# Optimization experiments

Hardware: AMD Instinct MI355X
Metric: run time of the kernel (lower is better)

## Reference

```python
import jax, jax.numpy as jnp
import numpy as np

B, N, DIM, HEADS, DH, EDGE, DEPTH, K = 4, 128, 256, 8, 64, 64, 2, 512
INNER = HEADS * DH
SCALE = DH ** -0.5


def _ln(x, g, b, eps=1e-5):
    m = x.mean(-1, keepdims=True)
    v = ((x - m) ** 2).mean(-1, keepdims=True)
    return (x - m) / jnp.sqrt(v + eps) * g + b


def _rotate_half(x):
    # interleaved pairs: (d r) with r=2 -> (-x2, x1)
    xp = x.reshape(x.shape[:-1] + (-1, 2))
    x1, x2 = xp[..., 0], xp[..., 1]
    return jnp.stack((-x2, x1), axis=-1).reshape(x.shape)


def _gated_res(x, res, gw):
    gate = jax.nn.sigmoid(jnp.concatenate((x, res, x - res), axis=-1) @ gw)
    return x * gate + res * (1 - gate)


def forward(nodes, edges, edge_ln_g, edge_ln_b, ln1_g, ln1_b, w_exp, b_exp,
            w_q, b_q, w_kv, b_kv, w_ekv, b_ekv, w_out, b_out, gate1_w,
            ln2_g, ln2_b, w_ff1, b_ff1, w_ff2, b_ff2, gate2_w, codebook):
    b, n = nodes.shape[:2]
    # LayerNorm edges over channel dim: (B,C,N,N) -> (B,N,N,C)
    e = _ln(jnp.transpose(edges, (0, 2, 3, 1)), edge_ln_g, edge_ln_b)
    # rotary frequencies over positions, repeated pairwise -> (1, N, DH)
    inv = 1.0 / (10000.0 ** (jnp.arange(0, DH, 2, dtype=jnp.float32) / DH))
    fr = jnp.repeat(jnp.arange(n, dtype=jnp.float32)[:, None] * inv[None, :], 2, axis=-1)
    cos, sin = jnp.cos(fr)[None], jnp.sin(fr)[None]

    def heads3(t):  # (B,N,H*D) -> (B*H,N,D)
        return t.reshape(b, n, HEADS, DH).transpose(0, 2, 1, 3).reshape(b * HEADS, n, DH)

    for i in range(DEPTH):
        # PreNorm + edge-conditioned attention
        x = _ln(nodes, ln1_g[i], ln1_b[i])
        x = x @ w_exp[i] + b_exp[i]
        q = x @ w_q[i] + b_q[i]
        k, v = jnp.split(x @ w_kv[i] + b_kv[i], 2, axis=-1)
        ekv = e @ w_ekv[i] + b_ekv[i]  # (B,N,N,INNER)
        q, k, v = heads3(q), heads3(k), heads3(v)
        ekv = ekv.reshape(b, n, n, HEADS, DH).transpose(0, 3, 1, 2, 4).reshape(b * HEADS, n, n, DH)
        q = q * cos + _rotate_half(q) * sin
        k = k * cos + _rotate_half(k) * sin
        kk = k[:, None, :, :] + ekv  # (BH, i, j, d)
        vv = v[:, None, :, :] + ekv
        sim = jnp.einsum('bid,bijd->bij', q, kk) * SCALE
        att = jax.nn.softmax(sim, axis=-1)
        out = jnp.einsum('bij,bijd->bid', att, vv)
        out = out.reshape(b, HEADS, n, DH).transpose(0, 2, 1, 3).reshape(b, n, INNER)
        out = out @ w_out[i] + b_out[i]
        nodes = _gated_res(out, nodes, gate1_w[i])
        # PreNorm + FeedForward
        h = _ln(nodes, ln2_g[i], ln2_b[i])
        h = jax.nn.gelu(h @ w_ff1[i] + b_ff1[i], approximate=False) @ w_ff2[i] + b_ff2[i]
        nodes = _gated_res(h, nodes, gate2_w[i])

    # VQ codebook nearest-neighbor lookup with straight-through estimator
    z = nodes.reshape(-1, DIM)
    d = (z * z).sum(-1, keepdims=True) - 2.0 * z @ codebook.T + (codebook * codebook).sum(-1)[None, :]
    idx = jnp.argmin(d, axis=-1)
    zq = codebook[idx].reshape(b, n, DIM)
    return nodes + jax.lax.stop_gradient(zq - nodes)


def setup_inputs() -> dict:
    key = jax.random.key(0)
    ks = jax.random.split(key, 16)
    s = 0.02
    inp = {
        'nodes': jax.random.normal(ks[0], (B, N, DIM), jnp.float32),
        'edges': jax.random.normal(ks[1], (B, EDGE, N, N), jnp.float32),
        'edge_ln_g': jnp.ones((EDGE,), jnp.float32),
        'edge_ln_b': jnp.zeros((EDGE,), jnp.float32),
        'ln1_g': jnp.ones((DEPTH, DIM), jnp.float32),
        'ln1_b': jnp.zeros((DEPTH, DIM), jnp.float32),
        'w_exp': s * jax.random.normal(ks[2], (DEPTH, DIM, INNER), jnp.float32),
        'b_exp': jnp.zeros((DEPTH, INNER), jnp.float32),
        'w_q': s * jax.random.normal(ks[3], (DEPTH, INNER, INNER), jnp.float32),
        'b_q': jnp.zeros((DEPTH, INNER), jnp.float32),
        'w_kv': s * jax.random.normal(ks[4], (DEPTH, INNER, 2 * INNER), jnp.float32),
        'b_kv': jnp.zeros((DEPTH, 2 * INNER), jnp.float32),
        'w_ekv': s * jax.random.normal(ks[5], (DEPTH, EDGE, INNER), jnp.float32),
        'b_ekv': jnp.zeros((DEPTH, INNER), jnp.float32),
        'w_out': s * jax.random.normal(ks[6], (DEPTH, INNER, DIM), jnp.float32),
        'b_out': jnp.zeros((DEPTH, DIM), jnp.float32),
        'gate1_w': s * jax.random.normal(ks[7], (DEPTH, 3 * DIM, 1), jnp.float32),
        'ln2_g': jnp.ones((DEPTH, DIM), jnp.float32),
        'ln2_b': jnp.zeros((DEPTH, DIM), jnp.float32),
        'w_ff1': s * jax.random.normal(ks[8], (DEPTH, DIM, 4 * DIM), jnp.float32),
        'b_ff1': jnp.zeros((DEPTH, 4 * DIM), jnp.float32),
        'w_ff2': s * jax.random.normal(ks[9], (DEPTH, 4 * DIM, DIM), jnp.float32),
        'b_ff2': jnp.zeros((DEPTH, DIM), jnp.float32),
        'gate2_w': s * jax.random.normal(ks[10], (DEPTH, 3 * DIM, 1), jnp.float32),
        'codebook': jax.random.uniform(ks[11], (K, DIM), jnp.float32, -1.0 / K, 1.0 / K),
    }
    return inp


def reference(nodes, edges, edge_ln_g, edge_ln_b, ln1_g, ln1_b, w_exp, b_exp,
              w_q, b_q, w_kv, b_kv, w_ekv, b_ekv, w_out, b_out, gate1_w,
              ln2_g, ln2_b, w_ff1, b_ff1, w_ff2, b_ff2, gate2_w, codebook):
    return forward(nodes, edges, edge_ln_g, edge_ln_b, ln1_g, ln1_b, w_exp, b_exp,
                   w_q, b_q, w_kv, b_kv, w_ekv, b_ekv, w_out, b_out, gate1_w,
                   ln2_g, ln2_b, w_ff1, b_ff1, w_ff2, b_ff2, gate2_w, codebook)
```

## Files before the change

### kernel.cpp

```cpp
#include <hip/hip_runtime.h>
#include <math.h>


#define DEV __device__ __forceinline__

constexpr int Bn = 4, Nn = 128, DIMn = 256, HEADSn = 8, DHn = 64, EDGEn = 64,
              DEPTHn = 2, Kn = 512, INNERn = 512;
constexpr int QKVW = 1536;
constexpr int PART = 131072;

DEV float wave_reduce_sum(float v) {
#pragma unroll
  for (int m = 32; m >= 1; m >>= 1) v += __shfl_xor(v, m);
  return v;
}

DEV float block_reduce_sum_256(float v, float* red) {
  v = wave_reduce_sum(v);
  int tid = threadIdx.x;
  if ((tid & 63) == 0) red[tid >> 6] = v;
  __syncthreads();
  v = red[0] + red[1] + red[2] + red[3];
  __syncthreads();
  return v;
}

DEV float gelu_exact(float x) {
  return 0.5f * x * (1.f + erff(x * 0.70710678118654752f));
}

__global__ __launch_bounds__(256) void prep_kernel(
    const float* __restrict__ edges, const float* __restrict__ eg,
    const float* __restrict__ eb, float* __restrict__ e,
    float* __restrict__ eT, float* __restrict__ cost, float* __restrict__ sint,
    const float* __restrict__ nodes_in, const float* __restrict__ ln1_g,
    const float* __restrict__ ln1_b, float* __restrict__ xln,
    float* __restrict__ nodes, const float* __restrict__ wek,
    const float* __restrict__ w_out, const float* __restrict__ bek,
    const float* __restrict__ b_out, float* __restrict__ W2,
    float* __restrict__ b_out2, const float* __restrict__ w_exp,
    const float* __restrict__ b_exp, const float* __restrict__ w_q,
    const float* __restrict__ b_q, const float* __restrict__ w_kv,
    const float* __restrict__ b_kv, float* __restrict__ WqkvF,
    float* __restrict__ bqkvF) {
  __shared__ float smem[8512];
  int blk = blockIdx.x;
  int tid = threadIdx.x;

  if (blk < 64) {
    int l = blk >> 5, h = (blk >> 2) & 7, nt = blk & 3;
    float* As = smem;
    float* Bs = smem + 4160;
    const float* wekl = wek + (size_t)l * 64 * 512 + h * 64;
    const float* woutl =
        w_out + (size_t)l * 512 * 256 + (size_t)(h * 64) * 256 + nt * 64;
    for (int f = tid; f < 1024; f += 256) {
      int c = f >> 4, d4 = (f & 15) << 2;
      float4 w4 = *(const float4*)(wekl + (size_t)c * 512 + d4);
      As[c * 65 + d4 + 0] = w4.x;
      As[c * 65 + d4 + 1] = w4.y;
      As[c * 65 + d4 + 2] = w4.z;
      As[c * 65 + d4 + 3] = w4.w;
    }
    for (int f = tid; f < 1024; f += 256) {
      int d = f >> 4, n4 = (f & 15) << 2;
      float4 w4 = *(const float4*)(woutl + (size_t)d * 256 + n4);
      Bs[d * 68 + n4 + 0] = w4.x;
      Bs[d * 68 + n4 + 1] = w4.y;
      Bs[d * 68 + n4 + 2] = w4.z;
      Bs[d * 68 + n4 + 3] = w4.w;
    }
    __syncthreads();
    int tx = tid & 15, ty = tid >> 4;
    float acc[4][4] = {};
    for (int d = 0; d < 64; ++d) {
      float4 bv = *(const float4*)&Bs[d * 68 + tx * 4];
#pragma unroll
      for (int u = 0; u < 4; ++u) {
        float a = As[(ty * 4 + u) * 65 + d];
        acc[u][0] += a * bv.x;
        acc[u][1] += a * bv.y;
        acc[u][2] += a * bv.z;
        acc[u][3] += a * bv.w;
      }
    }
#pragma unroll
    for (int u = 0; u < 4; ++u) {
      float4 o = {acc[u][0], acc[u][1], acc[u][2], acc[u][3]};
      *(float4*)(W2 + (size_t)l * 512 * 256 +
                 (size_t)(h * 64 + ty * 4 + u) * 256 + nt * 64 + tx * 4) = o;
    }
  } else if (blk < 72) {
    int t = blk - 64;
    int l = t >> 2, nt = t & 3;
    float* part = smem;
    int nn = tid & 63, kq = tid >> 6;
    const float* wcol = w_out + (size_t)l * 512 * 256 + nt * 64 + nn;
    float acc = 0.f;
    for (int k = kq * 128; k < kq * 128 + 128; ++k)
      acc += bek[l * 512 + k] * wcol[(size_t)k * 256];
    part[tid] = acc;
    __syncthreads();
    if (tid < 64)
      b_out2[l * 256 + nt * 64 + nn] =
          b_out[l * 256 + nt * 64 + nn] + part[nn] + part[64 + nn] +
          part[128 + nn] + part[192 + nn];
  } else if (blk < 584) {
    float* ets = smem;
    int eidx = blk - 72;
    int i = eidx & 127, b = eidx >> 7;
    int j = tid & 127;
    bool act = tid < 128;
    if (act) {
      const float* src = edges + (size_t)b * EDGEn * Nn * Nn + i * Nn + j;
      float vals[EDGEn];
      float s = 0.f;
#pragma unroll
      for (int c = 0; c < EDGEn; ++c) {
        float x = src[(size_t)c * (Nn * Nn)];
        vals[c] = x;
        s += x;
      }
      float m = s * (1.0f / 64.0f);
      float s2 = 0.f;
#pragma unroll
      for (int c = 0; c < EDGEn; ++c) {
        float d = vals[c] - m;
        s2 += d * d;
      }
      float inv = 1.f / sqrtf(s2 * (1.0f / 64.0f) + 1e-5f);
      float* dst = e + ((size_t)(b * Nn + i) * EDGEn) * Nn + j;
#pragma unroll
      for (int c = 0; c < EDGEn; ++c) {
        float o = (vals[c] - m) * inv * eg[c] + eb[c];
        dst[(size_t)c * Nn] = o;
        ets[j * 65 + c] = o;
      }
    }
    __syncthreads();
    if (act) {
      float* dstT = eT + ((size_t)(b * Nn + i) * Nn) * EDGEn;
#pragma unroll
      for (int it = 0; it < 16; ++it) {
        int f4 = it * 128 + j;
        int jj = f4 >> 4, c4 = (f4 & 15) << 2;
        float4 o4 = {ets[jj * 65 + c4], ets[jj * 65 + c4 + 1],
                     ets[jj * 65 + c4 + 2], ets[jj * 65 + c4 + 3]};
        *(float4*)(dstT + (size_t)jj * EDGEn + c4) = o4;
      }
    }
  } else if (blk < 600) {
    int t = (blk - 584) * 256 + tid;
    if (t < Nn * 32) {
      int n = t >> 5, p = t & 31;
      float inv = powf(10000.f, -(float)(2 * p) / 64.f);
      float fr = (float)n * inv;
      cost[t] = cosf(fr);
      sint[t] = sinf(fr);
    }
  } else if (blk < 1112) {
    float* red = smem;
    int row = blk - 600;
    float v = nodes_in[(size_t)row * DIMn + tid];
    nodes[(size_t)row * DIMn + tid] = v;
    float m = block_reduce_sum_256(v, red) * (1.0f / 256.0f);
    float d = v - m;
    float var = block_reduce_sum_256(d * d, red) * (1.0f / 256.0f);
    float inv = 1.f / sqrtf(var + 1e-5f);
    xln[(size_t)row * DIMn + tid] = d * inv * ln1_g[tid] + ln1_b[tid];
  } else if (blk < 1496) {
    int t = blk - 1112;
    int l = t / 192, r = t % 192;
    int by = r / 24, bx = r % 24;
    float* As = smem;
    float* Bs = smem + 32 * 34;
    int n0 = bx * 64;
    const float* Aab = w_exp + (size_t)l * 256 * 512 + (size_t)(by * 32) * 512;
    const float* Wb;
    int ldw;
    if (n0 < 512) {
      Wb = w_q + (size_t)l * 512 * 512 + n0;
      ldw = 512;
    } else {
      Wb = w_kv + (size_t)l * 512 * 1024 + (n0 - 512);
      ldw = 1024;
    }
    int arow = tid >> 3, acol = (tid & 7) << 2;
    int brow = tid >> 4, bcol = (tid & 15) << 2;
    int tx = tid & 15, ty = tid >> 4;
    float acc[2][4] = {};
    for (int k0 = 0; k0 < 512; k0 += 32) {
      float4 a4 = *(const float4*)(Aab + (size_t)arow * 512 + k0 + acol);
      As[(acol + 0) * 34 + arow] = a4.x;
      As[(acol + 1) * 34 + arow] = a4.y;
      As[(acol + 2) * 34 + arow] = a4.z;
      As[(acol + 3) * 34 + arow] = a4.w;
      *(float4*)&Bs[brow * 68 + bcol] =
          *(const float4*)(Wb + (size_t)(k0 + brow) * ldw + bcol);
      *(float4*)&Bs[(brow + 16) * 68 + bcol] =
          *(const float4*)(Wb + (size_t)(k0 + brow + 16) * ldw + bcol);
      __syncthreads();
#pragma unroll
      for (int kk = 0; kk < 32; ++kk) {
        float2 av = *(const float2*)&As[kk * 34 + ty * 2];
        float4 bv = *(const float4*)&Bs[kk * 68 + tx * 4];
        acc[0][0] += av.x * bv.x;
        acc[0][1] += av.x * bv.y;
        acc[0][2] += av.x * bv.z;
        acc[0][3] += av.x * bv.w;
        acc[1][0] += av.y * bv.x;
        acc[1][1] += av.y * bv.y;
        acc[1][2] += av.y * bv.z;
        acc[1][3] += av.y * bv.w;
      }
      __syncthreads();
    }
#pragma unroll
    for (int u = 0; u < 2; ++u) {
      int d = by * 32 + ty * 2 + u;
      float4 o = {acc[u][0], acc[u][1], acc[u][2], acc[u][3]};
      *(float4*)(WqkvF + (size_t)l * 256 * 1536 + (size_t)d * 1536 + n0 +
                 tx * 4) = o;
    }
  } else {
    int t = blk - 1496;
    int l = t / 6, seg = t % 6;
    int n = seg * 256 + tid;
    const float* W;
    int ldw;
    float acc;
    if (n < 512) {
      W = w_q + (size_t)l * 512 * 512 + n;
      ldw = 512;
      acc = b_q[l * 512 + n];
    } else {
      W = w_kv + (size_t)l * 512 * 1024 + (n - 512);
      ldw = 1024;
      acc = b_kv[l * 1024 + (n - 512)];
    }
    const float* be = b_exp + l * 512;
    for (int k = 0; k < 512; ++k) acc += be[k] * W[(size_t)k * ldw];
    bqkvF[l * 1536 + n] = acc;
  }
}

__global__ __launch_bounds__(256) void gemm_kernel(
    const float* __restrict__ A, const float* __restrict__ A2, int aact,
    const float* __restrict__ W1, int N1, const float* __restrict__ b1,
    const float* __restrict__ W2n, int N2, const float* __restrict__ b2,
    const float* __restrict__ Wkb, int Ksplit, float* __restrict__ C, int M,
    int Ntot, int K, int kspan, int act, const float* __restrict__ cost,
    const float* __restrict__ sint, float* __restrict__ kT) {
  __shared__ float As[32][34];
  __shared__ __align__(16) float Bs[32][68];
  int tid = threadIdx.x;
  int bx = blockIdx.x, by = blockIdx.y, zid = blockIdx.z;
  int tx = tid & 15, ty = tid >> 4;
  int arow = tid >> 3, acol = (tid & 7) << 2;
  int brow = tid >> 4, bcol = (tid & 15) << 2;
  int col0 = bx * 64;
  const float* W = W1;
  const float* bias = b1;
  int Nw = N1, wcol = col0;
  if (W2n && col0 >= N1) {
    W = W2n;
    bias = b2;
    Nw = N2;
    wcol = col0 - N1;
  }
  int kb = zid * kspan, kend = kb + kspan;
  const float* arp = A + (size_t)(by * 32 + arow) * K;
  const float* arp2 = A2 ? A2 + (size_t)(by * 32 + arow) * K : nullptr;

  auto load_a = [&](int kpos) -> float4 {
    float4 a = *(const float4*)(arp + kpos + acol);
    if (arp2) {
      float4 a2 = *(const float4*)(arp2 + kpos + acol);
      a.x += a2.x;
      a.y += a2.y;
      a.z += a2.z;
      a.w += a2.w;
    }
    if (aact == 1) {
      a.x = gelu_exact(a.x);
      a.y = gelu_exact(a.y);
      a.z = gelu_exact(a.z);
      a.w = gelu_exact(a.w);
    }
    return a;
  };

  float4 a_nxt = load_a(kb);
  const float* w0p;
  const float* w1p;
  {
    int kr0 = kb + brow, kr1 = kb + brow + 16;
    w0p = (Ksplit && kr0 >= Ksplit)
              ? Wkb + (size_t)(kr0 - Ksplit) * Nw + wcol + bcol
              : W + (size_t)kr0 * Nw + wcol + bcol;
    w1p = (Ksplit && kr1 >= Ksplit)
              ? Wkb + (size_t)(kr1 - Ksplit) * Nw + wcol + bcol
              : W + (size_t)kr1 * Nw + wcol + bcol;
  }
  float4 b0_nxt = *(const float4*)w0p;
  float4 b1_nxt = *(const float4*)w1p;

  float acc[2][4] = {};
  for (int k0 = kb; k0 < kend; k0 += 32) {
    As[acol + 0][arow] = a_nxt.x;
    As[acol + 1][arow] = a_nxt.y;
    As[acol + 2][arow] = a_nxt.z;
    As[acol + 3][arow] = a_nxt.w;
    *(float4*)&Bs[brow][bcol] = b0_nxt;
    *(float4*)&Bs[brow + 16][bcol] = b1_nxt;
    __syncthreads();
    int kn = k0 + 32;
    if (kn < kend) {
      a_nxt = load_a(kn);
      int kr0 = kn + brow, kr1 = kn + brow + 16;
      w0p = (Ksplit && kr0 >= Ksplit)
                ? Wkb + (size_t)(kr0 - Ksplit) * Nw + wcol + bcol
                : W + (size_t)kr0 * Nw + wcol + bcol;
      w1p = (Ksplit && kr1 >= Ksplit)
                ? Wkb + (size_t)(kr1 - Ksplit) * Nw + wcol + bcol
                : W + (size_t)kr1 * Nw + wcol + bcol;
      b0_nxt = *(const float4*)w0p;
      b1_nxt = *(const float4*)w1p;
    }
#pragma unroll
    for (int kk = 0; kk < 32; ++kk) {
      float2 av = *(const float2*)&As[kk][ty * 2];
      float4 bv = *(const float4*)&Bs[kk][tx * 4];
      acc[0][0] += av.x * bv.x;
      acc[0][1] += av.x * bv.y;
      acc[0][2] += av.x * bv.z;
      acc[0][3] += av.x * bv.w;
      acc[1][0] += av.y * bv.x;
      acc[1][1] += av.y * bv.y;
      acc[1][2] += av.y * bv.z;
      acc[1][3] += av.y * bv.w;
    }
    __syncthreads();
  }
  int ccol = wcol + tx * 4;
  bool ksec = (act == 4) && (col0 >= 512) && (col0 < 1024);
  float* trans = (float*)Bs;
  float* Cz = C + (size_t)zid * M * Ntot;
#pragma unroll
  for (int u = 0; u < 2; ++u) {
    int r = by * 32 + ty * 2 + u;
    float o[4];
#pragma unroll
    for (int w = 0; w < 4; ++w)
      o[w] = acc[u][w] + (zid == 0 ? bias[ccol + w] : 0.f);
    if (act == 1) {
#pragma unroll
      for (int w = 0; w < 4; ++w) o[w] = gelu_exact(o[w]);
    } else if (act == 4 && col0 < 1024) {
      int n = r & 127;
      int p0 = (ccol & 63) >> 1;
      float c0 = cost[n * 32 + p0], s0 = sint[n * 32 + p0];
      float c1 = cost[n * 32 + p0 + 1], s1 = sint[n * 32 + p0 + 1];
      float x0 = o[0], x1 = o[1], x2 = o[2], x3 = o[3];
      o[0] = x0 * c0 - x1 * s0;
      o[1] = x1 * c0 + x0 * s0;
      o[2] = x2 * c1 - x3 * s1;
      o[3] = x3 * c1 + x2 * s1;
    }
    if (ksec) {
#pragma unroll
      for (int w = 0; w < 4; ++w) trans[(tx * 4 + w) * 33 + ty * 2 + u] = o[w];
    } else {
      float4 o4 = {o[0], o[1], o[2], o[3]};
      *(float4*)(Cz + (size_t)r * Ntot + col0 + tx * 4) = o4;
    }
  }
  if (ksec) {
    __syncthreads();
    int h = (col0 - 512) >> 6;
    int bb = (by * 32) >> 7;
#pragma unroll
    for (int q = 0; q < 2; ++q) {
      int f4 = tid * 2 + q;
      int dl = f4 >> 3, j4 = (f4 & 7) << 2;
      int jj = (by * 32 + j4) & 127;
      float4 o4 = {trans[dl * 33 + j4], trans[dl * 33 + j4 + 1],
                   trans[dl * 33 + j4 + 2], trans[dl * 33 + j4 + 3]};
      *(float4*)(kT + ((size_t)(bb * 8 + h) * 64 + dl) * 128 + jj) = o4;
    }
  }
}

__global__ __launch_bounds__(128) void attn_kernel(
    const float* __restrict__ qkv, const float* __restrict__ e,
    const float* __restrict__ eT, const float* __restrict__ kT,
    const float* __restrict__ wek, const float* __restrict__ w_out,
    const float* __restrict__ W2, float* __restrict__ proj) {
  __shared__ __align__(16) float qs[256];
  __shared__ __align__(16) float qes[256];
  __shared__ __align__(16) float att[512];
  __shared__ float avh[512];
  __shared__ float aeh[512];
  __shared__ float wekh[64 * 65];
  int blk = blockIdx.x;
  int iq = blk & 31;
  int bh = blk >> 5;
  int h = bh & 7, b = bh >> 3;
  int i0 = iq * 4;
  int row0 = b * 128 + i0;
  int tid = threadIdx.x;

  for (int f = tid; f < 256; f += 128) {
    int ii = f >> 6, d = f & 63;
    qs[f] = qkv[(size_t)(row0 + ii) * QKVW + h * 64 + d];
  }
  for (int f = tid; f < 4096; f += 128) {
    int c = f >> 6, d = f & 63;
    wekh[c * 65 + d] = wek[(size_t)c * INNERn + h * 64 + d];
  }
  __syncthreads();

  for (int f = tid; f < 256; f += 128) {
    int ii = f >> 6, c = f & 63;
    float acc = 0.f;
#pragma unroll
    for (int d = 0; d < 64; ++d) acc += qs[ii * 64 + d] * wekh[c * 65 + d];
    qes[f] = acc;
  }
  __syncthreads();

  int i2 = tid >> 5, j4 = tid & 31;
  float s0 = 0.f, s1 = 0.f, s2 = 0.f, s3 = 0.f;
  {
    const float* ktb = kT + ((size_t)bh * 64) * 128 + j4 * 4;
#pragma unroll
    for (int d4 = 0; d4 < 64; d4 += 4) {
      float4 q4 = *(const float4*)&qs[i2 * 64 + d4];
      float4 k0 = *(const float4*)(ktb + (size_t)(d4 + 0) * 128);
      float4 k1 = *(const float4*)(ktb + (size_t)(d4 + 1) * 128);
      float4 k2 = *(const float4*)(ktb + (size_t)(d4 + 2) * 128);
      float4 k3 = *(const float4*)(ktb + (size_t)(d4 + 3) * 128);
      s0 += q4.x * k0.x + q4.y * k1.x + q4.z * k2.x + q4.w * k3.x;
      s1 += q4.x * k0.y + q4.y * k1.y + q4.z * k2.y + q4.w * k3.y;
      s2 += q4.x * k0.z + q4.y * k1.z + q4.z * k2.z + q4.w * k3.z;
      s3 += q4.x * k0.w + q4.y * k1.w + q4.z * k2.w + q4.w * k3.w;
    }
    const float* eb = e + ((size_t)(row0 + i2) * 64) * 128 + j4 * 4;
#pragma unroll
    for (int c4 = 0; c4 < 64; c4 += 4) {
      float4 qe4 = *(const float4*)&qes[i2 * 64 + c4];
      float4 e0 = *(const float4*)(eb + (size_t)(c4 + 0) * 128);
      float4 e1 = *(const float4*)(eb + (size_t)(c4 + 1) * 128);
      float4 e2 = *(const float4*)(eb + (size_t)(c4 + 2) * 128);
      float4 e3 = *(const float4*)(eb + (size_t)(c4 + 3) * 128);
      s0 += qe4.x * e0.x + qe4.y * e1.x + qe4.z * e2.x + qe4.w * e3.x;
      s1 += qe4.x * e0.y + qe4.y * e1.y + qe4.z * e2.y + qe4.w * e3.y;
      s2 += qe4.x * e0.z + qe4.y * e1.z + qe4.z * e2.z + qe4.w * e3.z;
      s3 += qe4.x * e0.w + qe4.y * e1.w + qe4.z * e2.w + qe4.w * e3.w;
    }
    s0 *= 0.125f;
    s1 *= 0.125f;
    s2 *= 0.125f;
    s3 *= 0.125f;
  }
  {
    float mx = fmaxf(fmaxf(s0, s1), fmaxf(s2, s3));
#pragma unroll
    for (int m = 16; m >= 1; m >>= 1) mx = fmaxf(mx, __shfl_xor(mx, m));
    float p0 = expf(s0 - mx), p1 = expf(s1 - mx), p2 = expf(s2 - mx),
          p3 = expf(s3 - mx);
    float sm = p0 + p1 + p2 + p3;
#pragma unroll
    for (int m = 16; m >= 1; m >>= 1) sm += __shfl_xor(sm, m);
    float inv = 1.f / sm;
    float4 a4 = {p0 * inv, p1 * inv, p2 * inv, p3 * inv};
    *(float4*)&att[i2 * 128 + j4 * 4] = a4;
  }
  __syncthreads();

  {
    int d = tid & 63, half = tid >> 6;
    float av0 = 0.f, av1 = 0.f, av2 = 0.f, av3 = 0.f;
    float ae0 = 0.f, ae1 = 0.f, ae2 = 0.f, ae3 = 0.f;
    const float* vb = qkv + (size_t)(b * 128) * QKVW + 1024 + h * 64 + d;
    const float* etb = eT + ((size_t)row0 * 128) * 64 + d;
    for (int jq = 0; jq < 16; ++jq) {
      int jb = half * 64 + jq * 4;
      float4 a0 = *(const float4*)&att[0 * 128 + jb];
      float4 a1 = *(const float4*)&att[1 * 128 + jb];
      float4 a2 = *(const float4*)&att[2 * 128 + jb];
      float4 a3 = *(const float4*)&att[3 * 128 + jb];
#pragma unroll
      for (int t = 0; t < 4; ++t) {
        int j = jb + t;
        float vv = vb[(size_t)j * QKVW];
        float at0 = ((const float*)&a0)[t];
        float at1 = ((const float*)&a1)[t];
        float at2 = ((const float*)&a2)[t];
        float at3 = ((const float*)&a3)[t];
        av0 += at0 * vv;
        av1 += at1 * vv;
        av2 += at2 * vv;
        av3 += at3 * vv;
        float e0 = etb[(size_t)j * 64];
        float e1 = etb[8192 + (size_t)j * 64];
        float e2 = etb[16384 + (size_t)j * 64];
        float e3 = etb[24576 + (size_t)j * 64];
        ae0 += at0 * e0;
        ae1 += at1 * e1;
        ae2 += at2 * e2;
        ae3 += at3 * e3;
      }
    }
    avh[half * 256 + 0 * 64 + d] = av0;
    avh[half * 256 + 1 * 64 + d] = av1;
    avh[half * 256 + 2 * 64 + d] = av2;
    avh[half * 256 + 3 * 64 + d] = av3;
    aeh[half * 256 + 0 * 64 + d] = ae0;
    aeh[half * 256 + 1 * 64 + d] = ae1;
    aeh[half * 256 + 2 * 64 + d] = ae2;
    aeh[half * 256 + 3 * 64 + d] = ae3;
  }
  __syncthreads();

  for (int f = tid; f < 256; f += 128) {
    int ii = f >> 6, dd = f & 63;
    att[ii * 128 + dd] = avh[ii * 64 + dd] + avh[256 + ii * 64 + dd];
    att[ii * 128 + 64 + dd] = aeh[ii * 64 + dd] + aeh[256 + ii * 64 + dd];
  }
  __syncthreads();

  {
    int rp = tid >> 6, n4 = (tid & 63) << 2;
    int r0 = rp * 2, r1 = rp * 2 + 1;
    float o0[4] = {}, o1[4] = {};
    const float* wo = w_out + (size_t)(h * 64) * 256 + n4;
#pragma unroll 8
    for (int k = 0; k < 64; ++k) {
      float4 w4 = *(const float4*)(wo + (size_t)k * 256);
      float a0 = att[r0 * 128 + k];
      float a1 = att[r1 * 128 + k];
      o0[0] += a0 * w4.x;
      o0[1] += a0 * w4.y;
      o0[2] += a0 * w4.z;
      o0[3] += a0 * w4.w;
      o1[0] += a1 * w4.x;
      o1[1] += a1 * w4.y;
      o1[2] += a1 * w4.z;
      o1[3] += a1 * w4.w;
    }
    const float* w2 = W2 + (size_t)(h * 64) * 256 + n4;
#pragma unroll 8
    for (int k = 0; k < 64; ++k) {
      float4 w4 = *(const float4*)(w2 + (size_t)k * 256);
      float a0 = att[r0 * 128 + 64 + k];
      float a1 = att[r1 * 128 + 64 + k];
      o0[0] += a0 * w4.x;
      o0[1] += a0 * w4.y;
      o0[2] += a0 * w4.z;
      o0[3] += a0 * w4.w;
      o1[0] += a1 * w4.x;
      o1[1] += a1 * w4.y;
      o1[2] += a1 * w4.z;
      o1[3] += a1 * w4.w;
    }
    float* pp = proj + (size_t)h * PART;
    float4 v0 = {o0[0], o0[1], o0[2], o0[3]};
    float4 v1 = {o1[0], o1[1], o1[2], o1[3]};
    *(float4*)(pp + (size_t)(row0 + r0) * 256 + n4) = v0;
    *(float4*)(pp + (size_t)(row0 + r1) * 256 + n4) = v1;
  }
}

__global__ __launch_bounds__(256) void gate_ln_kernel(
    const float* __restrict__ x, int nparts, const float* __restrict__ badd,
    float* __restrict__ nodes, const float* __restrict__ gw,
    const float* __restrict__ lng, const float* __restrict__ lnb,
    float* __restrict__ xln) {
  __shared__ float red[4];
  int row = blockIdx.x, tid = threadIdx.x;
  size_t off = (size_t)row * DIMn + tid;
  float xv = x[off];
  for (int p = 1; p < nparts; ++p) xv += x[off + (size_t)p * PART];
  if (badd) xv += badd[tid];
  float rv = nodes[off];
  float pv =
      xv * gw[tid] + rv * gw[DIMn + tid] + (xv - rv) * gw[2 * DIMn + tid];
  float ssum = block_reduce_sum_256(pv, red);
  float gsig = 1.f / (1.f + expf(-ssum));
  float nv = xv * gsig + rv * (1.f - gsig);
  nodes[off] = nv;
  if (lng) {
    float m = block_reduce_sum_256(nv, red) * (1.0f / 256.0f);
    float d = nv - m;
    float var = block_reduce_sum_256(d * d, red) * (1.0f / 256.0f);
    float inv = 1.f / sqrtf(var + 1e-5f);
    xln[off] = d * inv * lng[tid] + lnb[tid];
  }
}

__global__ __launch_bounds__(256) void vq_kernel(
    const float* __restrict__ nodes, const float* __restrict__ codebook,
    float* __restrict__ out) {
  __shared__ __align__(16) float zs[4 * 256];
  __shared__ float wval[4][4];
  __shared__ int widx[4][4];
  __shared__ int fidx[4];
  int row0 = blockIdx.x * 4;
  int tid = threadIdx.x;
  for (int f = tid; f < 1024; f += 256) zs[f] = nodes[(size_t)row0 * DIMn + f];
  __syncthreads();
  int k1 = tid, k2 = tid + 256;
  const float4* c1p = (const float4*)(codebook + (size_t)k1 * DIMn);
  const float4* c2p = (const float4*)(codebook + (size_t)k2 * DIMn);
  float dot[4][2] = {};
  float cc0 = 0.f, cc1 = 0.f;
#pragma unroll 8
  for (int d4 = 0; d4 < 64; ++d4) {
    float4 c1 = c1p[d4], c2 = c2p[d4];
    cc0 += c1.x * c1.x + c1.y * c1.y + c1.z * c1.z + c1.w * c1.w;
    cc1 += c2.x * c2.x + c2.y * c2.y + c2.z * c2.z + c2.w * c2.w;
#pragma unroll
    for (int r = 0; r < 4; ++r) {
      float4 z = *(const float4*)&zs[r * 256 + d4 * 4];
      dot[r][0] += c1.x * z.x + c1.y * z.y + c1.z * z.z + c1.w * z.w;
      dot[r][1] += c2.x * z.x + c2.y * z.y + c2.z * z.z + c2.w * z.w;
    }
  }
  int lane = tid & 63, w = tid >> 6;
#pragma unroll
  for (int r = 0; r < 4; ++r) {
    float bv = cc0 - 2.f * dot[r][0];
    int bi = k1;
    float v2 = cc1 - 2.f * dot[r][1];
    if (v2 < bv) {
      bv = v2;
      bi = k2;
    }
#pragma unroll
    for (int m = 32; m >= 1; m >>= 1) {
      float ov = __shfl_xor(bv, m);
      int oi = __shfl_xor(bi, m);
      if (ov < bv || (ov == bv && oi < bi)) {
        bv = ov;
        bi = oi;
      }
    }
    if (lane == 0) {
      wval[r][w] = bv;
      widx[r][w] = bi;
    }
  }
  __syncthreads();
  if (tid < 4) {
    float bb = wval[tid][0];
    int bi = widx[tid][0];
    for (int t = 1; t < 4; ++t)
      if (wval[tid][t] < bb || (wval[tid][t] == bb && widx[tid][t] < bi)) {
        bb = wval[tid][t];
        bi = widx[tid][t];
      }
    fidx[tid] = bi;
  }
  __syncthreads();
  for (int f = tid; f < 1024; f += 256) {
    int r = f >> 8, d = f & 255;
    float zv = zs[f];
    float zq = codebook[(size_t)fidx[r] * DIMn + d];
    out[(size_t)(row0 + r) * DIMn + d] = zv + (zq - zv);
  }
}

extern "C" void kernel_launch(void* const* d_in, const int* in_sizes, int n_in,
                              void* d_out, int out_size, void* d_ws,
                              size_t ws_size, hipStream_t stream) {
  const float* nodes_in = (const float*)d_in[0];
  const float* edges = (const float*)d_in[1];
  const float* edge_ln_g = (const float*)d_in[2];
  const float* edge_ln_b = (const float*)d_in[3];
  const float* ln1_g = (const float*)d_in[4];
  const float* ln1_b = (const float*)d_in[5];
  const float* w_exp = (const float*)d_in[6];
  const float* b_exp = (const float*)d_in[7];
  const float* w_q = (const float*)d_in[8];
  const float* b_q = (const float*)d_in[9];
  const float* w_kv = (const float*)d_in[10];
  const float* b_kv = (const float*)d_in[11];
  const float* w_ekv = (const float*)d_in[12];
  const float* b_ekv = (const float*)d_in[13];
  const float* w_out = (const float*)d_in[14];
  const float* b_out = (const float*)d_in[15];
  const float* gate1_w = (const float*)d_in[16];
  const float* ln2_g = (const float*)d_in[17];
  const float* ln2_b = (const float*)d_in[18];
  const float* w_ff1 = (const float*)d_in[19];
  const float* b_ff1 = (const float*)d_in[20];
  const float* w_ff2 = (const float*)d_in[21];
  const float* b_ff2 = (const float*)d_in[22];
  const float* gate2_w = (const float*)d_in[23];
  const float* codebook = (const float*)d_in[24];

  float* ws = (float*)d_ws;
  float* e_buf = ws;
  float* eT_buf = e_buf + 4194304;
  float* cost = eT_buf + 4194304;
  float* sint = cost + 4096;
  float* nodes = sint + 4096;
  float* xln = nodes + 131072;
  float* qkvb = xln + 131072;
  float* kTb = qkvb + 786432;
  float* proj = kTb + 262144;
  float* ff1 = proj + 1048576;
  float* W2buf = ff1 + 1048576;
  float* bout2 = W2buf + 262144;
  float* WqkvF = bout2 + 512;
  float* bqkvF = WqkvF + 786432;

  prep_kernel<<<1508, 256, 0, stream>>>(
      edges, edge_ln_g, edge_ln_b, e_buf, eT_buf, cost, sint, nodes_in, ln1_g,
      ln1_b, xln, nodes, w_ekv, w_out, b_ekv, b_out, W2buf, bout2, w_exp,
      b_exp, w_q, b_q, w_kv, b_kv, WqkvF, bqkvF);

  for (int l = 0; l < DEPTHn; ++l) {
    gemm_kernel<<<dim3(24, 16, 1), 256, 0, stream>>>(
        xln, nullptr, 0, WqkvF + (size_t)l * 256 * 1536, 1536,
        bqkvF + l * 1536, nullptr, 0, nullptr, nullptr, 0, qkvb, 512, QKVW,
        256, 256, 4, cost, sint, kTb);
    attn_kernel<<<1024, 128, 0, stream>>>(qkvb, e_buf, eT_buf, kTb,
                                          w_ekv + l * 64 * 512,
                                          w_out + l * 512 * 256,
                                          W2buf + l * 512 * 256, proj);
    gate_ln_kernel<<<512, 256, 0, stream>>>(
        proj, 8, bout2 + l * 256, nodes, gate1_w + l * 768, ln2_g + l * 256,
        ln2_b + l * 256, xln);
    gemm_kernel<<<dim3(16, 16, 2), 256, 0, stream>>>(
        xln, nullptr, 0, w_ff1 + l * 256 * 1024, 1024, b_ff1 + l * 1024,
        nullptr, 0, nullptr, nullptr, 0, ff1, 512, 1024, 256, 128, 0, cost,
        sint, nullptr);
    gemm_kernel<<<dim3(4, 16, 4), 256, 0, stream>>>(
        ff1, ff1 + 524288, 1, w_ff2 + l * 1024 * 256, 256, b_ff2 + l * 256,
        nullptr, 0, nullptr, nullptr, 0, proj, 512, 256, 1024, 256, 0, cost,
        sint, nullptr);
    const float* nlng = (l + 1 < DEPTHn) ? ln1_g + (l + 1) * 256 : nullptr;
    const float* nlnb = (l + 1 < DEPTHn) ? ln1_b + (l + 1) * 256 : nullptr;
    gate_ln_kernel<<<512, 256, 0, stream>>>(proj, 4, nullptr, nodes,
                                            gate2_w + l * 768, nlng, nlnb,
                                            xln);
  }
  vq_kernel<<<128, 256, 0, stream>>>(nodes, codebook, (float*)d_out);
}
```

Before: 338.0 us.

## Reorder prep kernel blocks, shrink shared memory, prefetch weight-fold GEMM tiles

The prep kernel's heterogeneous block roles are reordered so the long serial bias-fold and weight-fold GEMM blocks launch first and the short LayerNorm blocks run last. Shared memory per block drops from about 34KB to about 18KB by chunking the edge transpose and the W2 fold into 32-wide pieces, which should let more blocks stay resident per CU. The fused weight GEMM now register-prefetches the next k-tile of global loads while computing on the current one. The costs are extra barriers in the chunked loops and more live registers for the prefetch.

After: 319.0 us. -5.6%, faster.

```diff
diff --git a/kernel.cpp b/kernel.cpp
--- a/kernel.cpp
+++ b/kernel.cpp
@@ -43,133 +43,32 @@
     const float* __restrict__ b_q, const float* __restrict__ w_kv,
     const float* __restrict__ b_kv, float* __restrict__ WqkvF,
     float* __restrict__ bqkvF) {
-  __shared__ float smem[8512];
+  __shared__ __align__(16) float smem[4480];
   int blk = blockIdx.x;
   int tid = threadIdx.x;
 
-  if (blk < 64) {
-    int l = blk >> 5, h = (blk >> 2) & 7, nt = blk & 3;
-    float* As = smem;
-    float* Bs = smem + 4160;
-    const float* wekl = wek + (size_t)l * 64 * 512 + h * 64;
-    const float* woutl =
-        w_out + (size_t)l * 512 * 256 + (size_t)(h * 64) * 256 + nt * 64;
-    for (int f = tid; f < 1024; f += 256) {
-      int c = f >> 4, d4 = (f & 15) << 2;
-      float4 w4 = *(const float4*)(wekl + (size_t)c * 512 + d4);
-      As[c * 65 + d4 + 0] = w4.x;
-      As[c * 65 + d4 + 1] = w4.y;
-      As[c * 65 + d4 + 2] = w4.z;
-      As[c * 65 + d4 + 3] = w4.w;
-    }
-    for (int f = tid; f < 1024; f += 256) {
-      int d = f >> 4, n4 = (f & 15) << 2;
-      float4 w4 = *(const float4*)(woutl + (size_t)d * 256 + n4);
-      Bs[d * 68 + n4 + 0] = w4.x;
-      Bs[d * 68 + n4 + 1] = w4.y;
-      Bs[d * 68 + n4 + 2] = w4.z;
-      Bs[d * 68 + n4 + 3] = w4.w;
-    }
-    __syncthreads();
-    int tx = tid & 15, ty = tid >> 4;
-    float acc[4][4] = {};
-    for (int d = 0; d < 64; ++d) {
-      float4 bv = *(const float4*)&Bs[d * 68 + tx * 4];
-#pragma unroll
-      for (int u = 0; u < 4; ++u) {
-        float a = As[(ty * 4 + u) * 65 + d];
-        acc[u][0] += a * bv.x;
-        acc[u][1] += a * bv.y;
-        acc[u][2] += a * bv.z;
-        acc[u][3] += a * bv.w;
-      }
-    }
-#pragma unroll
-    for (int u = 0; u < 4; ++u) {
-      float4 o = {acc[u][0], acc[u][1], acc[u][2], acc[u][3]};
-      *(float4*)(W2 + (size_t)l * 512 * 256 +
-                 (size_t)(h * 64 + ty * 4 + u) * 256 + nt * 64 + tx * 4) = o;
-    }
-  } else if (blk < 72) {
-    int t = blk - 64;
-    int l = t >> 2, nt = t & 3;
-    float* part = smem;
-    int nn = tid & 63, kq = tid >> 6;
-    const float* wcol = w_out + (size_t)l * 512 * 256 + nt * 64 + nn;
-    float acc = 0.f;
-    for (int k = kq * 128; k < kq * 128 + 128; ++k)
-      acc += bek[l * 512 + k] * wcol[(size_t)k * 256];
-    part[tid] = acc;
-    __syncthreads();
-    if (tid < 64)
-      b_out2[l * 256 + nt * 64 + nn] =
-          b_out[l * 256 + nt * 64 + nn] + part[nn] + part[64 + nn] +
-          part[128 + nn] + part[192 + nn];
-  } else if (blk < 584) {
-    float* ets = smem;
-    int eidx = blk - 72;
-    int i = eidx & 127, b = eidx >> 7;
-    int j = tid & 127;
-    bool act = tid < 128;
-    if (act) {
-      const float* src = edges + (size_t)b * EDGEn * Nn * Nn + i * Nn + j;
-      float vals[EDGEn];
-      float s = 0.f;
-#pragma unroll
-      for (int c = 0; c < EDGEn; ++c) {
-        float x = src[(size_t)c * (Nn * Nn)];
-        vals[c] = x;
-        s += x;
-      }
-      float m = s * (1.0f / 64.0f);
-      float s2 = 0.f;
-#pragma unroll
-      for (int c = 0; c < EDGEn; ++c) {
-        float d = vals[c] - m;
-        s2 += d * d;
-      }
-      float inv = 1.f / sqrtf(s2 * (1.0f / 64.0f) + 1e-5f);
-      float* dst = e + ((size_t)(b * Nn + i) * EDGEn) * Nn + j;
-#pragma unroll
-      for (int c = 0; c < EDGEn; ++c) {
-        float o = (vals[c] - m) * inv * eg[c] + eb[c];
-        dst[(size_t)c * Nn] = o;
-        ets[j * 65 + c] = o;
-      }
-    }
-    __syncthreads();
-    if (act) {
-      float* dstT = eT + ((size_t)(b * Nn + i) * Nn) * EDGEn;
-#pragma unroll
-      for (int it = 0; it < 16; ++it) {
-        int f4 = it * 128 + j;
-        int jj = f4 >> 4, c4 = (f4 & 15) << 2;
-        float4 o4 = {ets[jj * 65 + c4], ets[jj * 65 + c4 + 1],
-                     ets[jj * 65 + c4 + 2], ets[jj * 65 + c4 + 3]};
-        *(float4*)(dstT + (size_t)jj * EDGEn + c4) = o4;
-      }
-    }
-  } else if (blk < 600) {
-    int t = (blk - 584) * 256 + tid;
-    if (t < Nn * 32) {
-      int n = t >> 5, p = t & 31;
-      float inv = powf(10000.f, -(float)(2 * p) / 64.f);
-      float fr = (float)n * inv;
-      cost[t] = cosf(fr);
-      sint[t] = sinf(fr);
-    }
-  } else if (blk < 1112) {
-    float* red = smem;
-    int row = blk - 600;
-    float v = nodes_in[(size_t)row * DIMn + tid];
-    nodes[(size_t)row * DIMn + tid] = v;
-    float m = block_reduce_sum_256(v, red) * (1.0f / 256.0f);
-    float d = v - m;
-    float var = block_reduce_sum_256(d * d, red) * (1.0f / 256.0f);
-    float inv = 1.f / sqrtf(var + 1e-5f);
-    xln[(size_t)row * DIMn + tid] = d * inv * ln1_g[tid] + ln1_b[tid];
-  } else if (blk < 1496) {
-    int t = blk - 1112;
+  if (blk < 12) {
+    int t = blk;
+    int l = t / 6, seg = t % 6;
+    int n = seg * 256 + tid;
+    const float* W;
+    int ldw;
+    float acc;
+    if (n < 512) {
+      W = w_q + (size_t)l * 512 * 512 + n;
+      ldw = 512;
+      acc = b_q[l * 512 + n];
+    } else {
+      W = w_kv + (size_t)l * 512 * 1024 + (n - 512);
+      ldw = 1024;
+      acc = b_kv[l * 1024 + (n - 512)];
+    }
+    const float* be = b_exp + l * 512;
+#pragma unroll 8
+    for (int k = 0; k < 512; ++k) acc += be[k] * W[(size_t)k * ldw];
+    bqkvF[l * 1536 + n] = acc;
+  } else if (blk < 396) {
+    int t = blk - 12;
     int l = t / 192, r = t % 192;
     int by = r / 24, bx = r % 24;
     float* As = smem;
@@ -188,18 +87,24 @@
     int arow = tid >> 3, acol = (tid & 7) << 2;
     int brow = tid >> 4, bcol = (tid & 15) << 2;
     int tx = tid & 15, ty = tid >> 4;
+    float4 a_nxt = *(const float4*)(Aab + (size_t)arow * 512 + acol);
+    float4 b0_nxt = *(const float4*)(Wb + (size_t)brow * ldw + bcol);
+    float4 b1_nxt = *(const float4*)(Wb + (size_t)(brow + 16) * ldw + bcol);
     float acc[2][4] = {};
     for (int k0 = 0; k0 < 512; k0 += 32) {
-      float4 a4 = *(const float4*)(Aab + (size_t)arow * 512 + k0 + acol);
-      As[(acol + 0) * 34 + arow] = a4.x;
-      As[(acol + 1) * 34 + arow] = a4.y;
-      As[(acol + 2) * 34 + arow] = a4.z;
-      As[(acol + 3) * 34 + arow] = a4.w;
-      *(float4*)&Bs[brow * 68 + bcol] =
-          *(const float4*)(Wb + (size_t)(k0 + brow) * ldw + bcol);
-      *(float4*)&Bs[(brow + 16) * 68 + bcol] =
-          *(const float4*)(Wb + (size_t)(k0 + brow + 16) * ldw + bcol);
+      As[(acol + 0) * 34 + arow] = a_nxt.x;
+      As[(acol + 1) * 34 + arow] = a_nxt.y;
+      As[(acol + 2) * 34 + arow] = a_nxt.z;
+      As[(acol + 3) * 34 + arow] = a_nxt.w;
+      *(float4*)&Bs[brow * 68 + bcol] = b0_nxt;
+      *(float4*)&Bs[(brow + 16) * 68 + bcol] = b1_nxt;
       __syncthreads();
+      int kn = k0 + 32;
+      if (kn < 512) {
+        a_nxt = *(const float4*)(Aab + (size_t)arow * 512 + kn + acol);
+        b0_nxt = *(const float4*)(Wb + (size_t)(kn + brow) * ldw + bcol);
+        b1_nxt = *(const float4*)(Wb + (size_t)(kn + brow + 16) * ldw + bcol);
+      }
 #pragma unroll
       for (int kk = 0; kk < 32; ++kk) {
         float2 av = *(const float2*)&As[kk * 34 + ty * 2];
@@ -222,25 +127,134 @@
       *(float4*)(WqkvF + (size_t)l * 256 * 1536 + (size_t)d * 1536 + n0 +
                  tx * 4) = o;
     }
+  } else if (blk < 908) {
+    float* ets = smem;
+    int eidx = blk - 396;
+    int i = eidx & 127, b = eidx >> 7;
+    int j = tid & 127;
+    bool act = tid < 128;
+    float vals[EDGEn];
+    float m = 0.f, inv = 0.f;
+    if (act) {
+      const float* src = edges + (size_t)b * EDGEn * Nn * Nn + i * Nn + j;
+      float s = 0.f;
+#pragma unroll
+      for (int c = 0; c < EDGEn; ++c) {
+        float x = src[(size_t)c * (Nn * Nn)];
+        vals[c] = x;
+        s += x;
+      }
+      m = s * (1.0f / 64.0f);
+      float s2 = 0.f;
+#pragma unroll
+      for (int c = 0; c < EDGEn; ++c) {
+        float d = vals[c] - m;
+        s2 += d * d;
+      }
+      inv = 1.f / sqrtf(s2 * (1.0f / 64.0f) + 1e-5f);
+    }
+    float* dst = e + ((size_t)(b * Nn + i) * EDGEn) * Nn + j;
+    float* dstT = eT + ((size_t)(b * Nn + i) * Nn) * EDGEn;
+#pragma unroll
+    for (int ch = 0; ch < 2; ++ch) {
+      if (act) {
+#pragma unroll
+        for (int cc = 0; cc < 32; ++cc) {
+          int c = ch * 32 + cc;
+          float o = (vals[c] - m) * inv * eg[c] + eb[c];
+          dst[(size_t)c * Nn] = o;
+          ets[j * 33 + cc] = o;
+        }
+      }
+      __syncthreads();
+      if (act) {
+#pragma unroll
+        for (int it = 0; it < 8; ++it) {
+          int f4 = it * 128 + j;
+          int jj = f4 >> 3, c4 = (f4 & 7) << 2;
+          float4 o4 = {ets[jj * 33 + c4], ets[jj * 33 + c4 + 1],
+                       ets[jj * 33 + c4 + 2], ets[jj * 33 + c4 + 3]};
+          *(float4*)(dstT + (size_t)jj * EDGEn + ch * 32 + c4) = o4;
+        }
+      }
+      __syncthreads();
+    }
+  } else if (blk < 972) {
+    int t = blk - 908;
+    int l = t >> 5, h = (t >> 2) & 7, nt = t & 3;
+    float* As = smem;
+    float* Bs = smem + 64 * 36;
+    const float* wekl = wek + (size_t)l * 64 * 512 + h * 64;
+    const float* woutl =
+        w_out + (size_t)l * 512 * 256 + (size_t)(h * 64) * 256 + nt * 64;
+    int tx = tid & 15, ty = tid >> 4;
+    float acc[4][4] = {};
+    for (int d0 = 0; d0 < 64; d0 += 32) {
+      for (int f = tid; f < 512; f += 256) {
+        int c = f >> 3, d4 = (f & 7) << 2;
+        *(float4*)&As[c * 36 + d4] =
+            *(const float4*)(wekl + (size_t)c * 512 + d0 + d4);
+      }
+      for (int f = tid; f < 512; f += 256) {
+        int dd = f >> 4, n4 = (f & 15) << 2;
+        *(float4*)&Bs[dd * 68 + n4] =
+            *(const float4*)(woutl + (size_t)(d0 + dd) * 256 + n4);
+      }
+      __syncthreads();
+#pragma unroll
+      for (int dd = 0; dd < 32; ++dd) {
+        float4 bv = *(const float4*)&Bs[dd * 68 + tx * 4];
+#pragma unroll
+        for (int u = 0; u < 4; ++u) {
+          float a = As[(ty * 4 + u) * 36 + dd];
+          acc[u][0] += a * bv.x;
+          acc[u][1] += a * bv.y;
+          acc[u][2] += a * bv.z;
+          acc[u][3] += a * bv.w;
+        }
+      }
+      __syncthreads();
+    }
+#pragma unroll
+    for (int u = 0; u < 4; ++u) {
+      float4 o = {acc[u][0], acc[u][1], acc[u][2], acc[u][3]};
+      *(float4*)(W2 + (size_t)l * 512 * 256 +
+                 (size_t)(h * 64 + ty * 4 + u) * 256 + nt * 64 + tx * 4) = o;
+    }
+  } else if (blk < 980) {
+    int t = blk - 972;
+    int l = t >> 2, nt = t & 3;
+    float* part = smem;
+    int nn = tid & 63, kq = tid >> 6;
+    const float* wcol = w_out + (size_t)l * 512 * 256 + nt * 64 + nn;
+    float acc = 0.f;
+    for (int k = kq * 128; k < kq * 128 + 128; ++k)
+      acc += bek[l * 512 + k] * wcol[(size_t)k * 256];
+    part[tid] = acc;
+    __syncthreads();
+    if (tid < 64)
+      b_out2[l * 256 + nt * 64 + nn] =
+          b_out[l * 256 + nt * 64 + nn] + part[nn] + part[64 + nn] +
+          part[128 + nn] + part[192 + nn];
+  } else if (blk < 996) {
+    int t = (blk - 980) * 256 + tid;
+    if (t < Nn * 32) {
+      int n = t >> 5, p = t & 31;
+      float inv = powf(10000.f, -(float)(2 * p) / 64.f);
+      float fr = (float)n * inv;
+      cost[t] = cosf(fr);
+      sint[t] = sinf(fr);
+    }
   } else {
-    int t = blk - 1496;
-    int l = t / 6, seg = t % 6;
-    int n = seg * 256 + tid;
-    const float* W;
-    int ldw;
-    float acc;
-    if (n < 512) {
-      W = w_q + (size_t)l * 512 * 512 + n;
-      ldw = 512;
-      acc = b_q[l * 512 + n];
-    } else {
-      W = w_kv + (size_t)l * 512 * 1024 + (n - 512);
-      ldw = 1024;
-      acc = b_kv[l * 1024 + (n - 512)];
-    }
-    const float* be = b_exp + l * 512;
-    for (int k = 0; k < 512; ++k) acc += be[k] * W[(size_t)k * ldw];
-    bqkvF[l * 1536 + n] = acc;
+    float* red = smem;
+    int row = blk - 996;
+    float v = nodes_in[(size_t)row * DIMn + tid];
+    nodes[(size_t)row * DIMn + tid] = v;
+    float m = block_reduce_sum_256(v, red) * (1.0f / 256.0f);
+    float d = v - m;
+    float var = block_reduce_sum_256(d * d, red) * (1.0f / 256.0f);
+    float inv = 1.f / sqrtf(var + 1e-5f);
+    xln[(size_t)row * DIMn + tid] = d * inv * ln1_g[tid] + ln1_b[tid];
   }
 }
 
```
